# Performance work log

Hardware: AMD Instinct MI355X
Metric: run time of the kernel (lower is better)

Reference implementation:

```python
import jax, jax.numpy as jnp
import numpy as np


def setup_inputs() -> dict:
    key = jax.random.key(0)
    k1, k2 = jax.random.split(key)
    x = jax.random.normal(k1, (32, 128, 56, 56), dtype=jnp.float32)
    weight = jax.random.normal(k2, (256, 128, 3, 3), dtype=jnp.float32) * 0.01
    bias = jnp.zeros((256,), dtype=jnp.float32)
    return {"x": x, "weight": weight, "bias": bias}


def reference(x, weight, bias):
    # Faithful to Conv2dGEMM: im2col + GEMM is mathematically a standard
    # cross-correlation conv with the given stride/padding. We express it as
    # the efficient fused form (implicit GEMM) which computes identical math.
    stride, padding = 1, 1
    out = jax.lax.conv_general_dilated(
        x, weight,
        window_strides=(stride, stride),
        padding=[(padding, padding), (padding, padding)],
        dimension_numbers=("NCHW", "OIHW", "NCHW"),
    )  # [B, out_ch, H_out, W_out]
    return out + bias[None, :, None, None]
```

## Files before the change

### kernel.cpp

```cpp
#include <hip/hip_runtime.h>
#include <stdint.h>

typedef __bf16 bf16x8 __attribute__((ext_vector_type(8)));
typedef float  f32x4  __attribute__((ext_vector_type(4)));

#define NB   32
#define CI   128
#define HH   56
#define WW   56
#define CO   256
#define HP   58
#define HW   (HH*WW)
#define MTOT (NB*HW)
#define KTOT 1152

#define XT_ELEMS ((size_t)NB*HP*HP*CI)
#define XT_BYTES (XT_ELEMS*2)

__global__ void halo_zero(__bf16* __restrict__ xt) {
  int id = blockIdx.x * 256 + threadIdx.x;
  if (id >= NB * 228 * 16) return;
  int chunk = id & 15;
  int p = (id >> 4) % 228;
  int n = id / (228 * 16);
  int h, w;
  if (p < 58)       { h = 0;           w = p; }
  else if (p < 116) { h = 57;          w = p - 58; }
  else if (p < 172) { h = p - 116 + 1; w = 0; }
  else              { h = p - 172 + 1; w = 57; }
  int4* dst = (int4*)(xt + ((size_t)(n * HP + h) * HP + w) * CI) + chunk;
  *dst = make_int4(0, 0, 0, 0);
}

__global__ void xpose_kernel(const float* __restrict__ x, __bf16* __restrict__ xt) {
  int nh = blockIdx.x;
  int n = nh / HH, h = nh % HH;
  __shared__ float tile[CI][57];
  const float* src = x + (size_t)n * CI * HW + (size_t)h * WW;
  int t = threadIdx.x;
  for (int idx = t; idx < CI * 14; idx += 256) {
    int c = idx / 14, w4 = idx - c * 14;
    float4 v = *(const float4*)(src + (size_t)c * HW + w4 * 4);
    tile[c][w4 * 4 + 0] = v.x;
    tile[c][w4 * 4 + 1] = v.y;
    tile[c][w4 * 4 + 2] = v.z;
    tile[c][w4 * 4 + 3] = v.w;
  }
  __syncthreads();
  __bf16* dst = xt + ((size_t)(n * HP + h + 1) * HP + 1) * CI;
  for (int idx = t; idx < WW * 16; idx += 256) {
    int w = idx >> 4, c8 = (idx & 15) * 8;
    bf16x8 v;
    for (int k = 0; k < 8; ++k) v[k] = (__bf16)tile[c8 + k][w];
    *(bf16x8*)(dst + (size_t)w * CI + c8) = v;
  }
}

__global__ void wxform_kernel(const float* __restrict__ wg, __bf16* __restrict__ wt) {
  int id = blockIdx.x * 256 + threadIdx.x;
  int o = id / KTOT;
  int k = id - o * KTOT;
  int rs = k >> 7, c = k & 127;
  wt[id] = (__bf16)wg[(size_t)o * KTOT + c * 9 + rs];
}

#define BM 128
#define BN 256
#define NKT 18

#define STAGE_A2(BS, OFF) \
  { _Pragma("unroll") for (int i_ = 0; i_ < 2; ++i_) \
      __builtin_amdgcn_global_load_lds( \
        (const __attribute__((address_space(1))) void*)(xtc + baseA[i_] + (OFF)), \
        (__attribute__((address_space(3))) void*)(lds + (BS)*16384 + i_*8192 + ldst), 16, 0, 0); }

#define STAGE_B01(BS, OFF) \
  { _Pragma("unroll") for (int i_ = 0; i_ < 2; ++i_) \
      __builtin_amdgcn_global_load_lds( \
        (const __attribute__((address_space(1))) void*)(wtc + baseB[i_] + (OFF)), \
        (__attribute__((address_space(3))) void*)(lds + 49152 + (BS)*32768 + i_*8192 + ldst), 16, 0, 0); }

#define STAGE_B23(BS, OFF) \
  { _Pragma("unroll") for (int i_ = 2; i_ < 4; ++i_) \
      __builtin_amdgcn_global_load_lds( \
        (const __attribute__((address_space(1))) void*)(wtc + baseB[i_] + (OFF)), \
        (__attribute__((address_space(3))) void*)(lds + 49152 + (BS)*32768 + i_*8192 + ldst), 16, 0, 0); }

#define KBODY(KT, BC, BS, DOSTAGE, DOBAR, VMCLIT) do { \
  int kt2_ = (KT) + 2; \
  int rs2_ = kt2_ >> 1; int r2_ = (rs2_*11)>>5; int s2_ = rs2_ - 3*r2_; \
  uint32_t offA2_ = (uint32_t)((r2_*HP + s2_) * 256 + (kt2_ & 1) * 128); \
  uint32_t offB2_ = (uint32_t)(kt2_ * 128); \
  const char* Ab_ = lds + (BC)*16384; \
  const char* Bb_ = lds + 49152 + (BC)*32768; \
  bf16x8 av_[4][2], bva_[2][2], bvb_[2][2]; \
  _Pragma("unroll") for (int a_ = 0; a_ < 4; ++a_) { \
    av_[a_][0] = *(const bf16x8*)(Ab_ + rowA + a_*2048 + slot0); \
    av_[a_][1] = *(const bf16x8*)(Ab_ + rowA + a_*2048 + slot1); } \
  _Pragma("unroll") for (int b_ = 0; b_ < 2; ++b_) { \
    bva_[b_][0] = *(const bf16x8*)(Bb_ + rowB + b_*2048 + slot0); \
    bva_[b_][1] = *(const bf16x8*)(Bb_ + rowB + b_*2048 + slot1); } \
  if (DOSTAGE) { STAGE_A2(BS, offA2_); STAGE_B01(BS, offB2_); } \
  __builtin_amdgcn_s_setprio(1); \
  _Pragma("unroll") for (int a_ = 0; a_ < 4; ++a_) { \
    _Pragma("unroll") for (int b_ = 0; b_ < 2; ++b_) { \
      acc[a_][b_] = __builtin_amdgcn_mfma_f32_16x16x32_bf16(av_[a_][0], bva_[b_][0], acc[a_][b_], 0, 0, 0); \
      acc[a_][b_] = __builtin_amdgcn_mfma_f32_16x16x32_bf16(av_[a_][1], bva_[b_][1], acc[a_][b_], 0, 0, 0); } } \
  __builtin_amdgcn_s_setprio(0); \
  _Pragma("unroll") for (int b_ = 0; b_ < 2; ++b_) { \
    bvb_[b_][0] = *(const bf16x8*)(Bb_ + rowB + 4096 + b_*2048 + slot0); \
    bvb_[b_][1] = *(const bf16x8*)(Bb_ + rowB + 4096 + b_*2048 + slot1); } \
  if (DOSTAGE) { STAGE_B23(BS, offB2_); } \
  __builtin_amdgcn_s_setprio(1); \
  _Pragma("unroll") for (int a_ = 0; a_ < 4; ++a_) { \
    _Pragma("unroll") for (int b_ = 0; b_ < 2; ++b_) { \
      acc[a_][b_+2] = __builtin_amdgcn_mfma_f32_16x16x32_bf16(av_[a_][0], bvb_[b_][0], acc[a_][b_+2], 0, 0, 0); \
      acc[a_][b_+2] = __builtin_amdgcn_mfma_f32_16x16x32_bf16(av_[a_][1], bvb_[b_][1], acc[a_][b_+2], 0, 0, 0); } } \
  __builtin_amdgcn_s_setprio(0); \
  if (DOBAR) { \
    asm volatile("s_waitcnt vmcnt(" VMCLIT ")" ::: "memory"); \
    __builtin_amdgcn_sched_barrier(0); \
    __builtin_amdgcn_s_barrier(); \
    __builtin_amdgcn_sched_barrier(0); } \
} while (0)

__global__ __launch_bounds__(512, 2) void conv_gemm(
    const __bf16* __restrict__ xt, const __bf16* __restrict__ wt,
    const float* __restrict__ bias, float* __restrict__ out) {
  __shared__ char lds[147456];
  int t = threadIdx.x;
  int mb = blockIdx.x;
  const char* xtc = (const char*)xt;
  const char* wtc = (const char*)wt;

  int arow = t >> 3;
  int kbsrc = ((t & 7) * 16) ^ ((arow & 7) << 4);
  int ldst = t * 16;
  uint32_t baseA[2];
#pragma unroll
  for (int i = 0; i < 2; ++i) {
    unsigned m = mb * BM + i * 64 + arow;
    unsigned nimg = m / HW;
    unsigned hw = m - nimg * HW;
    unsigned h = hw / WW;
    unsigned w = hw - h * WW;
    baseA[i] = ((nimg * HP + h) * HP + w) * (CI * 2) + kbsrc;
  }
  uint32_t baseB[4];
#pragma unroll
  for (int i = 0; i < 4; ++i)
    baseB[i] = (i * 64 + arow) * (KTOT * 2) + kbsrc;

  int wid = t >> 6, lane = t & 63;
  int wm = (wid >> 2) * 64;
  int wn = (wid & 3) * 64;
  int lr = lane & 15, hi = lane >> 4;
  int swz = (lr & 7) << 4;
  int slot0 = (hi * 16) ^ swz;
  int slot1 = (64 + hi * 16) ^ swz;
  int rowA = (wm + lr) * 128;
  int rowB = (wn + lr) * 128;

  f32x4 acc[4][4];
#pragma unroll
  for (int i = 0; i < 4; ++i)
#pragma unroll
    for (int j = 0; j < 4; ++j) acc[i][j] = (f32x4){0.f, 0.f, 0.f, 0.f};

  STAGE_A2(0, 0u);   STAGE_B01(0, 0u);   STAGE_B23(0, 0u);
  STAGE_A2(1, 128u); STAGE_B01(1, 128u); STAGE_B23(1, 128u);
  asm volatile("s_waitcnt vmcnt(6)" ::: "memory");
  __builtin_amdgcn_sched_barrier(0);
  __builtin_amdgcn_s_barrier();
  __builtin_amdgcn_sched_barrier(0);

  for (int kt = 0; kt < 15; kt += 3) {
    KBODY(kt + 0, 0, 2, 1, 1, "6");
    KBODY(kt + 1, 1, 0, 1, 1, "6");
    KBODY(kt + 2, 2, 1, 1, 1, "6");
  }
  KBODY(15, 0, 2, 1, 1, "6");
  KBODY(16, 1, 0, 0, 1, "0");
  KBODY(17, 2, 1, 0, 0, "0");

#pragma unroll
  for (int j = 0; j < 4; ++j) {
    int o = wn + j * 16 + lr;
    float bv = bias[o];
#pragma unroll
    for (int i = 0; i < 4; ++i) {
      unsigned m0 = mb * BM + wm + i * 16 + hi * 4;
      unsigned nimg = m0 / HW;
      unsigned hw = m0 - nimg * HW;
      f32x4 v = acc[i][j];
      v[0] += bv; v[1] += bv; v[2] += bv; v[3] += bv;
      *(f32x4*)(out + ((size_t)nimg * CO + o) * HW + hw) = v;
    }
  }
}

extern "C" void kernel_launch(void* const* d_in, const int* in_sizes, int n_in,
                              void* d_out, int out_size, void* d_ws, size_t ws_size,
                              hipStream_t stream) {
  const float* x    = (const float*)d_in[0];
  const float* wg   = (const float*)d_in[1];
  const float* bias = (const float*)d_in[2];
  float* out = (float*)d_out;

  __bf16* xt = (__bf16*)d_ws;
  __bf16* wt = (__bf16*)((char*)d_ws + XT_BYTES);

  halo_zero<<<(NB * 228 * 16 + 255) / 256, 256, 0, stream>>>(xt);
  xpose_kernel<<<NB * HH, 256, 0, stream>>>(x, xt);
  wxform_kernel<<<(CO * KTOT) / 256, 256, 0, stream>>>(wg, wt);
  conv_gemm<<<MTOT / BM, 512, 0, stream>>>(xt, wt, bias, out);
}
```

Before: 218.5 us.

## Split each K-tile into two half-K MFMA phases with barrier-synced LDS loads

Restructures each K-tile iteration into two phases that split the tile along K (slot0, then slot1) instead of along N. Each phase loads 4 A and 4 B fragments, issues part of the global-to-LDS staging, then does an s_barrier and a full lgkmcnt wait before a 16-MFMA burst. The aim is to lower register pressure and make the waves run the LDS-read and MFMA phases in lockstep, ping-pong style. In exchange it adds two extra workgroup barriers per K-tile and serialises the LDS reads ahead of the MFMAs, which could stall the waves.

After: 221.9 us. No clear change (+1.6%).

```diff
diff --git a/kernel.cpp b/kernel.cpp
--- a/kernel.cpp
+++ b/kernel.cpp
@@ -93,35 +93,47 @@
   uint32_t offB2_ = (uint32_t)(kt2_ * 128); \
   const char* Ab_ = lds + (BC)*16384; \
   const char* Bb_ = lds + 49152 + (BC)*32768; \
-  bf16x8 av_[4][2], bva_[2][2], bvb_[2][2]; \
-  _Pragma("unroll") for (int a_ = 0; a_ < 4; ++a_) { \
-    av_[a_][0] = *(const bf16x8*)(Ab_ + rowA + a_*2048 + slot0); \
-    av_[a_][1] = *(const bf16x8*)(Ab_ + rowA + a_*2048 + slot1); } \
-  _Pragma("unroll") for (int b_ = 0; b_ < 2; ++b_) { \
-    bva_[b_][0] = *(const bf16x8*)(Bb_ + rowB + b_*2048 + slot0); \
-    bva_[b_][1] = *(const bf16x8*)(Bb_ + rowB + b_*2048 + slot1); } \
-  if (DOSTAGE) { STAGE_A2(BS, offA2_); STAGE_B01(BS, offB2_); } \
-  __builtin_amdgcn_s_setprio(1); \
-  _Pragma("unroll") for (int a_ = 0; a_ < 4; ++a_) { \
-    _Pragma("unroll") for (int b_ = 0; b_ < 2; ++b_) { \
-      acc[a_][b_] = __builtin_amdgcn_mfma_f32_16x16x32_bf16(av_[a_][0], bva_[b_][0], acc[a_][b_], 0, 0, 0); \
-      acc[a_][b_] = __builtin_amdgcn_mfma_f32_16x16x32_bf16(av_[a_][1], bva_[b_][1], acc[a_][b_], 0, 0, 0); } } \
-  __builtin_amdgcn_s_setprio(0); \
-  _Pragma("unroll") for (int b_ = 0; b_ < 2; ++b_) { \
-    bvb_[b_][0] = *(const bf16x8*)(Bb_ + rowB + 4096 + b_*2048 + slot0); \
-    bvb_[b_][1] = *(const bf16x8*)(Bb_ + rowB + 4096 + b_*2048 + slot1); } \
-  if (DOSTAGE) { STAGE_B23(BS, offB2_); } \
-  __builtin_amdgcn_s_setprio(1); \
-  _Pragma("unroll") for (int a_ = 0; a_ < 4; ++a_) { \
-    _Pragma("unroll") for (int b_ = 0; b_ < 2; ++b_) { \
-      acc[a_][b_+2] = __builtin_amdgcn_mfma_f32_16x16x32_bf16(av_[a_][0], bvb_[b_][0], acc[a_][b_+2], 0, 0, 0); \
-      acc[a_][b_+2] = __builtin_amdgcn_mfma_f32_16x16x32_bf16(av_[a_][1], bvb_[b_][1], acc[a_][b_+2], 0, 0, 0); } } \
-  __builtin_amdgcn_s_setprio(0); \
-  if (DOBAR) { \
-    asm volatile("s_waitcnt vmcnt(" VMCLIT ")" ::: "memory"); \
+   \
+  { \
+    bf16x8 av_[4], bv_[4]; \
+    _Pragma("unroll") for (int a_ = 0; a_ < 4; ++a_) \
+      av_[a_] = *(const bf16x8*)(Ab_ + rowA + a_*2048 + slot0); \
+    _Pragma("unroll") for (int b_ = 0; b_ < 4; ++b_) \
+      bv_[b_] = *(const bf16x8*)(Bb_ + rowB + b_*2048 + slot0); \
+    if (DOSTAGE) { STAGE_A2(BS, offA2_); STAGE_B01(BS, offB2_); } \
+    __builtin_amdgcn_s_barrier(); \
+    asm volatile("s_waitcnt lgkmcnt(0)" ::: "memory"); \
     __builtin_amdgcn_sched_barrier(0); \
+    __builtin_amdgcn_s_setprio(1); \
+    _Pragma("unroll") for (int a_ = 0; a_ < 4; ++a_) \
+      _Pragma("unroll") for (int b_ = 0; b_ < 4; ++b_) \
+        acc[a_][b_] = __builtin_amdgcn_mfma_f32_16x16x32_bf16(av_[a_], bv_[b_], acc[a_][b_], 0, 0, 0); \
+    __builtin_amdgcn_s_setprio(0); \
     __builtin_amdgcn_s_barrier(); \
-    __builtin_amdgcn_sched_barrier(0); } \
+  } \
+   \
+  { \
+    bf16x8 av_[4], bv_[4]; \
+    _Pragma("unroll") for (int a_ = 0; a_ < 4; ++a_) \
+      av_[a_] = *(const bf16x8*)(Ab_ + rowA + a_*2048 + slot1); \
+    _Pragma("unroll") for (int b_ = 0; b_ < 4; ++b_) \
+      bv_[b_] = *(const bf16x8*)(Bb_ + rowB + b_*2048 + slot1); \
+    if (DOSTAGE) { STAGE_B23(BS, offB2_); } \
+    __builtin_amdgcn_s_barrier(); \
+    asm volatile("s_waitcnt lgkmcnt(0)" ::: "memory"); \
+    __builtin_amdgcn_sched_barrier(0); \
+    __builtin_amdgcn_s_setprio(1); \
+    _Pragma("unroll") for (int a_ = 0; a_ < 4; ++a_) \
+      _Pragma("unroll") for (int b_ = 0; b_ < 4; ++b_) \
+        acc[a_][b_] = __builtin_amdgcn_mfma_f32_16x16x32_bf16(av_[a_], bv_[b_], acc[a_][b_], 0, 0, 0); \
+    __builtin_amdgcn_s_setprio(0); \
+    if (DOBAR) { \
+      asm volatile("s_waitcnt vmcnt(" VMCLIT ")" ::: "memory"); \
+      __builtin_amdgcn_sched_barrier(0); \
+      __builtin_amdgcn_s_barrier(); \
+      __builtin_amdgcn_sched_barrier(0); \
+    } \
+  } \
 } while (0)
 
 __global__ __launch_bounds__(512, 2) void conv_gemm(
```

## Fuse prep kernels into one launch and make conv GEMM persistent with atomic tile queue

Applied to the files above, without the earlier changes.

Merges the halo-zero, input transpose and weight transform kernels into a single prep kernel that also resets a work counter. The GEMM kernel becomes persistent with 256 blocks that grab M tiles through an atomic counter, replacing the one-block-per-tile grid. The aim is to cut launch overhead and the tail effect of 784 tiles over the CUs. The cost is an extra atomic and __syncthreads per tile, and the loop no longer overlaps one tile's epilogue with the next tile's prologue loads.

Result: no change. 218.8 us (+0.2%).

```diff
diff --git a/kernel.cpp b/kernel.cpp
--- a/kernel.cpp
+++ b/kernel.cpp
@@ -16,57 +16,63 @@
 
 #define XT_ELEMS ((size_t)NB*HP*HP*CI)
 #define XT_BYTES (XT_ELEMS*2)
-
-__global__ void halo_zero(__bf16* __restrict__ xt) {
-  int id = blockIdx.x * 256 + threadIdx.x;
-  if (id >= NB * 228 * 16) return;
-  int chunk = id & 15;
-  int p = (id >> 4) % 228;
-  int n = id / (228 * 16);
-  int h, w;
-  if (p < 58)       { h = 0;           w = p; }
-  else if (p < 116) { h = 57;          w = p - 58; }
-  else if (p < 172) { h = p - 116 + 1; w = 0; }
-  else              { h = p - 172 + 1; w = 57; }
-  int4* dst = (int4*)(xt + ((size_t)(n * HP + h) * HP + w) * CI) + chunk;
-  *dst = make_int4(0, 0, 0, 0);
-}
-
-__global__ void xpose_kernel(const float* __restrict__ x, __bf16* __restrict__ xt) {
-  int nh = blockIdx.x;
-  int n = nh / HH, h = nh % HH;
+#define WT_BYTES ((size_t)CO*KTOT*2)
+#define CTR_OFF  (XT_BYTES + WT_BYTES)
+
+#define XPOSE_BLOCKS (NB*HH)
+#define WX_BLOCKS    ((CO*KTOT)/256)
+#define HALO_BLOCKS  ((NB*228*16)/256)
+
+__global__ void prep_kernel(const float* __restrict__ x, const float* __restrict__ wg,
+                            __bf16* __restrict__ xt, __bf16* __restrict__ wt,
+                            unsigned* __restrict__ ctr) {
   __shared__ float tile[CI][57];
-  const float* src = x + (size_t)n * CI * HW + (size_t)h * WW;
-  int t = threadIdx.x;
-  for (int idx = t; idx < CI * 14; idx += 256) {
-    int c = idx / 14, w4 = idx - c * 14;
-    float4 v = *(const float4*)(src + (size_t)c * HW + w4 * 4);
-    tile[c][w4 * 4 + 0] = v.x;
-    tile[c][w4 * 4 + 1] = v.y;
-    tile[c][w4 * 4 + 2] = v.z;
-    tile[c][w4 * 4 + 3] = v.w;
+  int bx = blockIdx.x, t = threadIdx.x;
+  if (bx == 0 && t == 0) *ctr = 0u;
+  if (bx < XPOSE_BLOCKS) {
+    int n = bx / HH, h = bx % HH;
+    const float* src = x + (size_t)n * CI * HW + (size_t)h * WW;
+    for (int idx = t; idx < CI * 14; idx += 256) {
+      int c = idx / 14, w4 = idx - c * 14;
+      float4 v = *(const float4*)(src + (size_t)c * HW + w4 * 4);
+      tile[c][w4 * 4 + 0] = v.x;
+      tile[c][w4 * 4 + 1] = v.y;
+      tile[c][w4 * 4 + 2] = v.z;
+      tile[c][w4 * 4 + 3] = v.w;
+    }
+    __syncthreads();
+    __bf16* dst = xt + ((size_t)(n * HP + h + 1) * HP + 1) * CI;
+    for (int idx = t; idx < WW * 16; idx += 256) {
+      int w = idx >> 4, c8 = (idx & 15) * 8;
+      bf16x8 v;
+      for (int k = 0; k < 8; ++k) v[k] = (__bf16)tile[c8 + k][w];
+      *(bf16x8*)(dst + (size_t)w * CI + c8) = v;
+    }
+  } else if (bx < XPOSE_BLOCKS + WX_BLOCKS) {
+    int id = (bx - XPOSE_BLOCKS) * 256 + t;
+    int o = id / KTOT;
+    int k = id - o * KTOT;
+    int rs = k >> 7, c = k & 127;
+    wt[id] = (__bf16)wg[(size_t)o * KTOT + c * 9 + rs];
+  } else {
+    int id = (bx - XPOSE_BLOCKS - WX_BLOCKS) * 256 + t;
+    int chunk = id & 15;
+    int p = (id >> 4) % 228;
+    int n = id / (228 * 16);
+    int h, w;
+    if (p < 58)       { h = 0;           w = p; }
+    else if (p < 116) { h = 57;          w = p - 58; }
+    else if (p < 172) { h = p - 116 + 1; w = 0; }
+    else              { h = p - 172 + 1; w = 57; }
+    int4* dst = (int4*)(xt + ((size_t)(n * HP + h) * HP + w) * CI) + chunk;
+    *dst = make_int4(0, 0, 0, 0);
   }
-  __syncthreads();
-  __bf16* dst = xt + ((size_t)(n * HP + h + 1) * HP + 1) * CI;
-  for (int idx = t; idx < WW * 16; idx += 256) {
-    int w = idx >> 4, c8 = (idx & 15) * 8;
-    bf16x8 v;
-    for (int k = 0; k < 8; ++k) v[k] = (__bf16)tile[c8 + k][w];
-    *(bf16x8*)(dst + (size_t)w * CI + c8) = v;
-  }
-}
-
-__global__ void wxform_kernel(const float* __restrict__ wg, __bf16* __restrict__ wt) {
-  int id = blockIdx.x * 256 + threadIdx.x;
-  int o = id / KTOT;
-  int k = id - o * KTOT;
-  int rs = k >> 7, c = k & 127;
-  wt[id] = (__bf16)wg[(size_t)o * KTOT + c * 9 + rs];
 }
 
 #define BM 128
 #define BN 256
 #define NKT 18
+#define NTILES (MTOT/BM)
 
 #define STAGE_A2(BS, OFF) \
   { _Pragma("unroll") for (int i_ = 0; i_ < 2; ++i_) \
@@ -88,7 +94,7 @@
 
 #define KBODY(KT, BC, BS, DOSTAGE, DOBAR, VMCLIT) do { \
   int kt2_ = (KT) + 2; \
-  int rs2_ = kt2_ >> 1; int r2_ = (rs2_*11)>>5; int s2_ = rs2_ - 3*r2_; \
+  int rs2_ = kt2_ >> 1; int r2_ = (rs2_*11) >> 5; int s2_ = rs2_ - 3*r2_; \
   uint32_t offA2_ = (uint32_t)((r2_*HP + s2_) * 256 + (kt2_ & 1) * 128); \
   uint32_t offB2_ = (uint32_t)(kt2_ * 128); \
   const char* Ab_ = lds + (BC)*16384; \
@@ -126,26 +132,17 @@
 
 __global__ __launch_bounds__(512, 2) void conv_gemm(
     const __bf16* __restrict__ xt, const __bf16* __restrict__ wt,
-    const float* __restrict__ bias, float* __restrict__ out) {
+    const float* __restrict__ bias, float* __restrict__ out,
+    unsigned* __restrict__ ctr) {
   __shared__ char lds[147456];
+  __shared__ int sh_mb;
   int t = threadIdx.x;
-  int mb = blockIdx.x;
   const char* xtc = (const char*)xt;
   const char* wtc = (const char*)wt;
 
   int arow = t >> 3;
   int kbsrc = ((t & 7) * 16) ^ ((arow & 7) << 4);
   int ldst = t * 16;
-  uint32_t baseA[2];
-#pragma unroll
-  for (int i = 0; i < 2; ++i) {
-    unsigned m = mb * BM + i * 64 + arow;
-    unsigned nimg = m / HW;
-    unsigned hw = m - nimg * HW;
-    unsigned h = hw / WW;
-    unsigned w = hw - h * WW;
-    baseA[i] = ((nimg * HP + h) * HP + w) * (CI * 2) + kbsrc;
-  }
   uint32_t baseB[4];
 #pragma unroll
   for (int i = 0; i < 4; ++i)
@@ -161,40 +158,58 @@
   int rowA = (wm + lr) * 128;
   int rowB = (wn + lr) * 128;
 
-  f32x4 acc[4][4];
-#pragma unroll
-  for (int i = 0; i < 4; ++i)
-#pragma unroll
-    for (int j = 0; j < 4; ++j) acc[i][j] = (f32x4){0.f, 0.f, 0.f, 0.f};
-
-  STAGE_A2(0, 0u);   STAGE_B01(0, 0u);   STAGE_B23(0, 0u);
-  STAGE_A2(1, 128u); STAGE_B01(1, 128u); STAGE_B23(1, 128u);
-  asm volatile("s_waitcnt vmcnt(6)" ::: "memory");
-  __builtin_amdgcn_sched_barrier(0);
-  __builtin_amdgcn_s_barrier();
-  __builtin_amdgcn_sched_barrier(0);
-
-  for (int kt = 0; kt < 15; kt += 3) {
-    KBODY(kt + 0, 0, 2, 1, 1, "6");
-    KBODY(kt + 1, 1, 0, 1, 1, "6");
-    KBODY(kt + 2, 2, 1, 1, 1, "6");
-  }
-  KBODY(15, 0, 2, 1, 1, "6");
-  KBODY(16, 1, 0, 0, 1, "0");
-  KBODY(17, 2, 1, 0, 0, "0");
-
-#pragma unroll
-  for (int j = 0; j < 4; ++j) {
-    int o = wn + j * 16 + lr;
-    float bv = bias[o];
-#pragma unroll
-    for (int i = 0; i < 4; ++i) {
-      unsigned m0 = mb * BM + wm + i * 16 + hi * 4;
-      unsigned nimg = m0 / HW;
-      unsigned hw = m0 - nimg * HW;
-      f32x4 v = acc[i][j];
-      v[0] += bv; v[1] += bv; v[2] += bv; v[3] += bv;
-      *(f32x4*)(out + ((size_t)nimg * CO + o) * HW + hw) = v;
+  for (;;) {
+    if (t == 0) sh_mb = (int)atomicAdd(ctr, 1u);
+    __syncthreads();
+    int mb = sh_mb;
+    if (mb >= NTILES) break;
+
+    uint32_t baseA[2];
+#pragma unroll
+    for (int i = 0; i < 2; ++i) {
+      unsigned m = mb * BM + i * 64 + arow;
+      unsigned nimg = m / HW;
+      unsigned hw = m - nimg * HW;
+      unsigned h = hw / WW;
+      unsigned w = hw - h * WW;
+      baseA[i] = ((nimg * HP + h) * HP + w) * (CI * 2) + kbsrc;
+    }
+
+    f32x4 acc[4][4];
+#pragma unroll
+    for (int i = 0; i < 4; ++i)
+#pragma unroll
+      for (int j = 0; j < 4; ++j) acc[i][j] = (f32x4){0.f, 0.f, 0.f, 0.f};
+
+    STAGE_A2(0, 0u);   STAGE_B01(0, 0u);   STAGE_B23(0, 0u);
+    STAGE_A2(1, 128u); STAGE_B01(1, 128u); STAGE_B23(1, 128u);
+    asm volatile("s_waitcnt vmcnt(6)" ::: "memory");
+    __builtin_amdgcn_sched_barrier(0);
+    __builtin_amdgcn_s_barrier();
+    __builtin_amdgcn_sched_barrier(0);
+
+    for (int kt = 0; kt < 15; kt += 3) {
+      KBODY(kt + 0, 0, 2, 1, 1, "6");
+      KBODY(kt + 1, 1, 0, 1, 1, "6");
+      KBODY(kt + 2, 2, 1, 1, 1, "6");
+    }
+    KBODY(15, 0, 2, 1, 1, "6");
+    KBODY(16, 1, 0, 0, 1, "0");
+    KBODY(17, 2, 1, 0, 0, "0");
+
+#pragma unroll
+    for (int j = 0; j < 4; ++j) {
+      int o = wn + j * 16 + lr;
+      float bv = bias[o];
+#pragma unroll
+      for (int i = 0; i < 4; ++i) {
+        unsigned m0 = mb * BM + wm + i * 16 + hi * 4;
+        unsigned nimg = m0 / HW;
+        unsigned hw = m0 - nimg * HW;
+        f32x4 v = acc[i][j];
+        v[0] += bv; v[1] += bv; v[2] += bv; v[3] += bv;
+        *(f32x4*)(out + ((size_t)nimg * CO + o) * HW + hw) = v;
+      }
     }
   }
 }
@@ -209,9 +224,8 @@
 
   __bf16* xt = (__bf16*)d_ws;
   __bf16* wt = (__bf16*)((char*)d_ws + XT_BYTES);
-
-  halo_zero<<<(NB * 228 * 16 + 255) / 256, 256, 0, stream>>>(xt);
-  xpose_kernel<<<NB * HH, 256, 0, stream>>>(x, xt);
-  wxform_kernel<<<(CO * KTOT) / 256, 256, 0, stream>>>(wg, wt);
-  conv_gemm<<<MTOT / BM, 512, 0, stream>>>(xt, wt, bias, out);
+  unsigned* ctr = (unsigned*)((char*)d_ws + CTR_OFF);
+
+  prep_kernel<<<XPOSE_BLOCKS + WX_BLOCKS + HALO_BLOCKS, 256, 0, stream>>>(x, wg, xt, wt, ctr);
+  conv_gemm<<<256, 512, 0, stream>>>(xt, wt, bias, out, ctr);
 }
```
